# Kernel tuning notes

Hardware: AMD Instinct MI355X
Metric: run time of the kernel (lower is better)

## Reference

```python
import jax, jax.numpy as jnp
import numpy as np

N = 4096


def setup_inputs() -> dict:
    key = jax.random.key(0)
    ks = jax.random.split(key, 24)

    def idx(k, n, cols):
        base = jax.random.randint(k, (n,), 0, N)
        return jnp.stack([(base + j) % N for j in range(cols)], axis=1).astype(jnp.int32)

    x = jax.random.normal(ks[0], (N, 3), jnp.float32) * 3.0  # spread points so min pair dist is not tiny
    bond = idx(ks[1], 6144, 2)
    kb = jax.random.uniform(ks[2], (6144,), jnp.float32)
    b0 = jax.random.uniform(ks[3], (6144,), jnp.float32)
    angle = idx(ks[4], 8192, 3)
    kt = jax.random.uniform(ks[5], (8192,), jnp.float32)
    t0 = jax.random.uniform(ks[6], (8192,), jnp.float32) * 180.0  # degrees
    ureybradley = idx(ks[7], 4096, 2)
    ku = jax.random.uniform(ks[8], (4096,), jnp.float32)
    s0 = jax.random.uniform(ks[9], (4096,), jnp.float32)
    dihedral = idx(ks[10], 12288, 4)
    kd = jax.random.uniform(ks[11], (12288,), jnp.float32)
    nd = jax.random.randint(ks[12], (12288,), 1, 4).astype(jnp.float32)  # multiplicity
    d0 = jax.random.uniform(ks[13], (12288,), jnp.float32) * 360.0
    improper = idx(ks[14], 2048, 4)
    kp = jax.random.uniform(ks[15], (2048,), jnp.float32)
    p0 = jax.random.uniform(ks[16], (2048,), jnp.float32) * 180.0
    eps_ij = jax.random.uniform(ks[17], (N, N), jnp.float32)
    rmin_ij = jax.random.uniform(ks[18], (N, N), jnp.float32) * 0.5
    kqq_ij = jax.random.normal(ks[19], (N, N), jnp.float32)
    return dict(x=x, kb=kb, b0=b0, kt=kt, t0=t0, ku=ku, s0=s0, kd=kd, nd=nd, d0=d0,
                kp=kp, p0=p0, eps_ij=eps_ij, rmin_ij=rmin_ij, kqq_ij=kqq_ij,
                bond=bond, angle=angle, ureybradley=ureybradley,
                dihedral=dihedral, improper=improper, central=0)


def _torsion(x, quad):
    # signed dihedral angle for [M,4] index quadruples
    ab = x[quad[:, 1]] - x[quad[:, 0]]
    bc = x[quad[:, 2]] - x[quad[:, 1]]
    cd = x[quad[:, 3]] - x[quad[:, 2]]
    n1 = jnp.cross(ab, bc)
    n2 = jnp.cross(bc, cd)
    cos_d = jnp.sum(n1 * n2, axis=1) / (jnp.linalg.norm(n1, axis=1) * jnp.linalg.norm(n2, axis=1))
    ang = jnp.arccos(jnp.clip(cos_d, -0.9999, 0.9999))
    return ang * jnp.sign(jnp.sum(jnp.cross(n1, n2) * bc, axis=1))


def _energy(x, kb, b0, kt, t0, ku, s0, kd, nd, d0, kp, p0,
            eps_ij, rmin_ij, kqq_ij, bond, angle, ureybradley, dihedral, improper, central):
    # bonds
    dis = jnp.linalg.norm(x[bond[:, 0]] - x[bond[:, 1]], axis=1)
    V_bond = jnp.sum(kb * (dis - b0) ** 2)
    # angles
    ba = x[angle[:, 0]] - x[angle[:, 1]]
    bc = x[angle[:, 2]] - x[angle[:, 1]]
    cos_t = jnp.sum(ba * bc, axis=1) / (jnp.linalg.norm(ba, axis=1) * jnp.linalg.norm(bc, axis=1))
    theta = jnp.arccos(jnp.clip(cos_t, -0.9999, 0.9999))
    V_angle = jnp.sum(kt * (theta - jnp.deg2rad(t0)) ** 2)
    # Urey-Bradley 1-3 terms
    dub = jnp.linalg.norm(x[ureybradley[:, 0]] - x[ureybradley[:, 1]], axis=1)
    V_ub = jnp.sum(ku * (dub - s0) ** 2)
    # proper dihedrals
    delta = _torsion(x, dihedral)
    V_dih = jnp.sum(kd * (1.0 + jnp.cos(nd * delta - jnp.deg2rad(d0))))
    # impropers (harmonic)
    psi = _torsion(x, improper)
    V_imp = jnp.sum(kp * (psi - jnp.deg2rad(p0)) ** 2)
    # nonbonded: cdist(x,x) + I, summed over strict upper triangle
    n = x.shape[0]
    sq = jnp.sum(x * x, axis=1)
    d2 = jnp.maximum(sq[:, None] + sq[None, :] - 2.0 * (x @ x.T), 1e-12)
    eye = jnp.eye(n, dtype=bool)
    dist = jnp.sqrt(jnp.where(eye, 1.0, d2))  # diag -> 1, matching cdist + eye
    rod = rmin_ij / dist
    vdw = eps_ij * (rod ** 12 - 2.0 * rod ** 6)
    mask = jnp.triu(jnp.ones((n, n), bool), 1)
    V_vdw = jnp.sum(jnp.where(mask, vdw, 0.0))
    V_ele = jnp.sum(jnp.where(mask, kqq_ij / dist, 0.0))
    V = V_bond + V_angle + V_ub + V_dih + V_imp + V_vdw + V_ele
    if central:
        V = V + jnp.sum(0.1 * jnp.sum((x - jnp.mean(x, axis=0)) ** 2, axis=1))
    return V


def reference(x, kb, b0, kt, t0, ku, s0, kd, nd, d0, kp, p0,
              eps_ij, rmin_ij, kqq_ij, bond, angle, ureybradley, dihedral, improper, central):
    return _energy(x, kb, b0, kt, t0, ku, s0, kd, nd, d0, kp, p0,
                   eps_ij, rmin_ij, kqq_ij, bond, angle, ureybradley, dihedral, improper, central)
```

## Files before the change

### kernel.cpp

```cpp
#include <hip/hip_runtime.h>

#define NATOM   4096
#define NG4     (NATOM / 4)
#define NBOND   6144
#define NANGLE  8192
#define NUB     4096
#define NDIH    12288
#define NIMP    2048

#define NB_BLOCKS   2048
#define BOND_ITEMS  (NBOND + NANGLE + NUB + NDIH + NIMP)
#define BOND_WORKB  (BOND_ITEMS / 256)
#define BOND_BLOCKS (BOND_WORKB + 1)
#define TOTAL_SLOTS (NB_BLOCKS + BOND_BLOCKS)

#define DEG2RAD 0.017453292519943295f

static __device__ __forceinline__ double block_reduce(double v, double* sm) {
    #pragma unroll
    for (int off = 32; off > 0; off >>= 1) v += __shfl_down(v, off, 64);
    const int lane = threadIdx.x & 63, wid = threadIdx.x >> 6;
    __syncthreads();
    if (lane == 0) sm[wid] = v;
    __syncthreads();
    double r = 0.0;
    if (threadIdx.x == 0) {
        const int nw = blockDim.x >> 6;
        for (int w = 0; w < nw; ++w) r += sm[w];
    }
    return r;
}

static __device__ __forceinline__ float pair_term(
    float xi0, float xi1, float xi2,
    float xj0, float xj1, float xj2,
    float e, float r, float q, bool valid)
{
    const float dx = xi0 - xj0, dy = xi1 - xj1, dz = xi2 - xj2;
    float d2 = fmaf(dx, dx, fmaf(dy, dy, dz * dz));
    d2 = fmaxf(d2, 1e-12f);
    float inv = rsqrtf(d2);
    const float t = inv * inv;
    inv = inv * fmaf(-0.5f * d2, t, 1.5f);
    const float rod = r * inv;
    const float r2 = rod * rod;
    const float r6 = r2 * r2 * r2;
    const float v = fmaf(e * r6, r6 - 2.0f, q * inv);
    return valid ? v : 0.0f;
}

__global__ __launch_bounds__(256) void nb_kernel(
    const float4* __restrict__ xv,
    const float4* __restrict__ eps,
    const float4* __restrict__ rmin,
    const float4* __restrict__ kqq,
    double* __restrict__ ws)
{
    __shared__ double sm[4];
    const float* __restrict__ xf = (const float*)xv;
    double acc = 0.0;
    #pragma unroll
    for (int half = 0; half < 2; ++half) {
        const int i = (half == 0) ? (int)blockIdx.x : (NATOM - 1 - (int)blockIdx.x);
        const float xi0 = xf[3*i], xi1 = xf[3*i+1], xi2 = xf[3*i+2];
        const int g0 = (i + 1) >> 2;
        const size_t rowbase = (size_t)i * NG4;
        for (int g = g0 + (int)threadIdx.x; g < NG4; g += 256) {
            const float4 e = eps [rowbase + g];
            const float4 r = rmin[rowbase + g];
            const float4 q = kqq [rowbase + g];
            const float4 xa = xv[3*g], xb = xv[3*g+1], xc = xv[3*g+2];
            const int j0 = 4 * g;
            float s;
            s  = pair_term(xi0,xi1,xi2, xa.x,xa.y,xa.z, e.x,r.x,q.x, j0+0 > i);
            s += pair_term(xi0,xi1,xi2, xa.w,xb.x,xb.y, e.y,r.y,q.y, j0+1 > i);
            s += pair_term(xi0,xi1,xi2, xb.z,xb.w,xc.x, e.z,r.z,q.z, j0+2 > i);
            s += pair_term(xi0,xi1,xi2, xc.y,xc.z,xc.w, e.w,r.w,q.w, j0+3 > i);
            acc += (double)s;
        }
    }
    const double tot = block_reduce(acc, sm);
    if (threadIdx.x == 0) ws[blockIdx.x] = tot;
}

static __device__ __forceinline__ float torsion(const float* __restrict__ x,
                                                int i0, int i1, int i2, int i3) {
    const float ax = x[3*i1] - x[3*i0], ay = x[3*i1+1] - x[3*i0+1], az = x[3*i1+2] - x[3*i0+2];
    const float bx = x[3*i2] - x[3*i1], by = x[3*i2+1] - x[3*i1+1], bz = x[3*i2+2] - x[3*i1+2];
    const float cx = x[3*i3] - x[3*i2], cy = x[3*i3+1] - x[3*i2+1], cz = x[3*i3+2] - x[3*i2+2];
    const float n1x = ay*bz - az*by, n1y = az*bx - ax*bz, n1z = ax*by - ay*bx;
    const float n2x = by*cz - bz*cy, n2y = bz*cx - bx*cz, n2z = bx*cy - by*cx;
    const float dt  = n1x*n2x + n1y*n2y + n1z*n2z;
    const float nn1 = sqrtf(n1x*n1x + n1y*n1y + n1z*n1z);
    const float nn2 = sqrtf(n2x*n2x + n2y*n2y + n2z*n2z);
    float c = dt / (nn1 * nn2);
    c = fminf(fmaxf(c, -0.9999f), 0.9999f);
    const float ang = acosf(c);
    const float sx = n1y*n2z - n1z*n2y, sy = n1z*n2x - n1x*n2z, sz = n1x*n2y - n1y*n2x;
    const float s = sx*bx + sy*by + sz*bz;
    const float sg = (s > 0.0f) ? 1.0f : ((s < 0.0f) ? -1.0f : 0.0f);
    return ang * sg;
}

__global__ __launch_bounds__(256) void bonded_kernel(
    const float* __restrict__ x,
    const float* __restrict__ kb, const float* __restrict__ b0,
    const float* __restrict__ kt, const float* __restrict__ t0,
    const float* __restrict__ ku, const float* __restrict__ s0,
    const float* __restrict__ kd, const float* __restrict__ nd, const float* __restrict__ d0,
    const float* __restrict__ kp, const float* __restrict__ p0,
    const int* __restrict__ bond, const int* __restrict__ angle,
    const int* __restrict__ ub,   const int* __restrict__ dih,
    const int* __restrict__ imp,  const int* __restrict__ central,
    double* __restrict__ ws)
{
    __shared__ double sm[4];

    if (blockIdx.x == BOND_WORKB) {
        double out = 0.0;
        if (*central != 0) {
            double sx = 0.0, sy = 0.0, sz = 0.0, s2 = 0.0;
            for (int i = threadIdx.x; i < NATOM; i += 256) {
                const float a = x[3*i], b = x[3*i+1], c = x[3*i+2];
                sx += a; sy += b; sz += c;
                s2 += (double)a*a + (double)b*b + (double)c*c;
            }
            const double rx = block_reduce(sx, sm);
            const double ry = block_reduce(sy, sm);
            const double rz = block_reduce(sz, sm);
            const double r2 = block_reduce(s2, sm);
            if (threadIdx.x == 0)
                out = 0.1 * (r2 - (rx*rx + ry*ry + rz*rz) / (double)NATOM);
        }
        if (threadIdx.x == 0) ws[NB_BLOCKS + blockIdx.x] = out;
        return;
    }

    const int t = (int)blockIdx.x * 256 + (int)threadIdx.x;
    double v = 0.0;

    if (t < NBOND) {
        const int m = t;
        const int i = bond[2*m], j = bond[2*m+1];
        const float dx = x[3*i]-x[3*j], dy = x[3*i+1]-x[3*j+1], dz = x[3*i+2]-x[3*j+2];
        const float dis = sqrtf(dx*dx + dy*dy + dz*dz);
        const float d = dis - b0[m];
        v = (double)(kb[m] * d * d);
    } else if (t < NBOND + NANGLE) {
        const int m = t - NBOND;
        const int i = angle[3*m], j = angle[3*m+1], k = angle[3*m+2];
        const float bax = x[3*i]-x[3*j], bay = x[3*i+1]-x[3*j+1], baz = x[3*i+2]-x[3*j+2];
        const float bcx = x[3*k]-x[3*j], bcy = x[3*k+1]-x[3*j+1], bcz = x[3*k+2]-x[3*j+2];
        const float dt  = bax*bcx + bay*bcy + baz*bcz;
        const float na  = sqrtf(bax*bax + bay*bay + baz*baz);
        const float nb  = sqrtf(bcx*bcx + bcy*bcy + bcz*bcz);
        float c = dt / (na * nb);
        c = fminf(fmaxf(c, -0.9999f), 0.9999f);
        const float theta = acosf(c);
        const float d = theta - t0[m] * DEG2RAD;
        v = (double)(kt[m] * d * d);
    } else if (t < NBOND + NANGLE + NUB) {
        const int m = t - NBOND - NANGLE;
        const int i = ub[2*m], j = ub[2*m+1];
        const float dx = x[3*i]-x[3*j], dy = x[3*i+1]-x[3*j+1], dz = x[3*i+2]-x[3*j+2];
        const float dis = sqrtf(dx*dx + dy*dy + dz*dz);
        const float d = dis - s0[m];
        v = (double)(ku[m] * d * d);
    } else if (t < NBOND + NANGLE + NUB + NDIH) {
        const int m = t - NBOND - NANGLE - NUB;
        const float delta = torsion(x, dih[4*m], dih[4*m+1], dih[4*m+2], dih[4*m+3]);
        v = (double)(kd[m] * (1.0f + cosf(nd[m] * delta - d0[m] * DEG2RAD)));
    } else {
        const int m = t - NBOND - NANGLE - NUB - NDIH;
        const float psi = torsion(x, imp[4*m], imp[4*m+1], imp[4*m+2], imp[4*m+3]);
        const float d = psi - p0[m] * DEG2RAD;
        v = (double)(kp[m] * d * d);
    }

    const double tot = block_reduce(v, sm);
    if (threadIdx.x == 0) ws[NB_BLOCKS + blockIdx.x] = tot;
}

__global__ __launch_bounds__(256) void finalize_kernel(const double* __restrict__ ws,
                                                       float* __restrict__ out) {
    __shared__ double sm[4];
    double v = 0.0;
    for (int i = threadIdx.x; i < TOTAL_SLOTS; i += 256) v += ws[i];
    const double tot = block_reduce(v, sm);
    if (threadIdx.x == 0) out[0] = (float)tot;
}

extern "C" void kernel_launch(void* const* d_in, const int* in_sizes, int n_in,
                              void* d_out, int out_size, void* d_ws, size_t ws_size,
                              hipStream_t stream) {
    const float* x    = (const float*)d_in[0];
    const float* kb   = (const float*)d_in[1];
    const float* b0   = (const float*)d_in[2];
    const float* kt   = (const float*)d_in[3];
    const float* t0   = (const float*)d_in[4];
    const float* ku   = (const float*)d_in[5];
    const float* s0   = (const float*)d_in[6];
    const float* kd   = (const float*)d_in[7];
    const float* nd   = (const float*)d_in[8];
    const float* d0   = (const float*)d_in[9];
    const float* kp   = (const float*)d_in[10];
    const float* p0   = (const float*)d_in[11];
    const float* eps  = (const float*)d_in[12];
    const float* rmin = (const float*)d_in[13];
    const float* kqq  = (const float*)d_in[14];
    const int* bond   = (const int*)d_in[15];
    const int* angle  = (const int*)d_in[16];
    const int* ub     = (const int*)d_in[17];
    const int* dih    = (const int*)d_in[18];
    const int* imp    = (const int*)d_in[19];
    const int* cent   = (const int*)d_in[20];

    double* ws = (double*)d_ws;

    nb_kernel<<<NB_BLOCKS, 256, 0, stream>>>((const float4*)x, (const float4*)eps,
                                             (const float4*)rmin, (const float4*)kqq, ws);
    bonded_kernel<<<BOND_BLOCKS, 256, 0, stream>>>(x, kb, b0, kt, t0, ku, s0,
                                                   kd, nd, d0, kp, p0,
                                                   bond, angle, ub, dih, imp, cent, ws);
    finalize_kernel<<<1, 256, 0, stream>>>(ws, (float*)d_out);
}
```

Baseline: 218.8 us.

## Fuse nonbonded and bonded kernels, flatten paired-row work into fixed per-thread loads

Merges the nonbonded and bonded energy kernels into one launch, where the first block range handles nonbonded row pairs and the rest handles bonded terms. Each nonbonded block now concatenates its two rows (i and N-1-i) into one work list of about 1024 float4 groups. Each thread issues four independent loads up front, replacing the strided loop with its divergent tail. The aim is to remove a launch, balance work across threads and raise memory-level parallelism. One thread handles a single leftover group when the combined count is 1025.

```diff
diff --git a/kernel.cpp b/kernel.cpp
--- a/kernel.cpp
+++ b/kernel.cpp
@@ -49,38 +49,17 @@
     return valid ? v : 0.0f;
 }
 
-__global__ __launch_bounds__(256) void nb_kernel(
-    const float4* __restrict__ xv,
-    const float4* __restrict__ eps,
-    const float4* __restrict__ rmin,
-    const float4* __restrict__ kqq,
-    double* __restrict__ ws)
+static __device__ __forceinline__ float group_term(
+    int i, float xi0, float xi1, float xi2, int g,
+    float4 e, float4 r, float4 q, float4 xa, float4 xb, float4 xc)
 {
-    __shared__ double sm[4];
-    const float* __restrict__ xf = (const float*)xv;
-    double acc = 0.0;
-    #pragma unroll
-    for (int half = 0; half < 2; ++half) {
-        const int i = (half == 0) ? (int)blockIdx.x : (NATOM - 1 - (int)blockIdx.x);
-        const float xi0 = xf[3*i], xi1 = xf[3*i+1], xi2 = xf[3*i+2];
-        const int g0 = (i + 1) >> 2;
-        const size_t rowbase = (size_t)i * NG4;
-        for (int g = g0 + (int)threadIdx.x; g < NG4; g += 256) {
-            const float4 e = eps [rowbase + g];
-            const float4 r = rmin[rowbase + g];
-            const float4 q = kqq [rowbase + g];
-            const float4 xa = xv[3*g], xb = xv[3*g+1], xc = xv[3*g+2];
-            const int j0 = 4 * g;
-            float s;
-            s  = pair_term(xi0,xi1,xi2, xa.x,xa.y,xa.z, e.x,r.x,q.x, j0+0 > i);
-            s += pair_term(xi0,xi1,xi2, xa.w,xb.x,xb.y, e.y,r.y,q.y, j0+1 > i);
-            s += pair_term(xi0,xi1,xi2, xb.z,xb.w,xc.x, e.z,r.z,q.z, j0+2 > i);
-            s += pair_term(xi0,xi1,xi2, xc.y,xc.z,xc.w, e.w,r.w,q.w, j0+3 > i);
-            acc += (double)s;
-        }
-    }
-    const double tot = block_reduce(acc, sm);
-    if (threadIdx.x == 0) ws[blockIdx.x] = tot;
+    const int j0 = 4 * g;
+    float s;
+    s  = pair_term(xi0,xi1,xi2, xa.x,xa.y,xa.z, e.x,r.x,q.x, j0+0 > i);
+    s += pair_term(xi0,xi1,xi2, xa.w,xb.x,xb.y, e.y,r.y,q.y, j0+1 > i);
+    s += pair_term(xi0,xi1,xi2, xb.z,xb.w,xc.x, e.z,r.z,q.z, j0+2 > i);
+    s += pair_term(xi0,xi1,xi2, xc.y,xc.z,xc.w, e.w,r.w,q.w, j0+3 > i);
+    return s;
 }
 
 static __device__ __forceinline__ float torsion(const float* __restrict__ x,
@@ -102,8 +81,11 @@
     return ang * sg;
 }
 
-__global__ __launch_bounds__(256) void bonded_kernel(
-    const float* __restrict__ x,
+__global__ __launch_bounds__(256) void ff_kernel(
+    const float4* __restrict__ xv,
+    const float4* __restrict__ eps,
+    const float4* __restrict__ rmin,
+    const float4* __restrict__ kqq,
     const float* __restrict__ kb, const float* __restrict__ b0,
     const float* __restrict__ kt, const float* __restrict__ t0,
     const float* __restrict__ ku, const float* __restrict__ s0,
@@ -115,8 +97,62 @@
     double* __restrict__ ws)
 {
     __shared__ double sm[4];
-
-    if (blockIdx.x == BOND_WORKB) {
+    const float* __restrict__ x = (const float*)xv;
+
+    if (blockIdx.x < NB_BLOCKS) {
+        const int b  = (int)blockIdx.x;
+        const int i0 = b, i1 = NATOM - 1 - b;
+        const float xi00 = x[3*i0], xi01 = x[3*i0+1], xi02 = x[3*i0+2];
+        const float xi10 = x[3*i1], xi11 = x[3*i1+1], xi12 = x[3*i1+2];
+        const int ga = (i0 + 1) >> 2, gb = (i1 + 1) >> 2;
+        const int c0 = NG4 - ga;
+        const int c1 = NG4 - gb;
+        const int total = c0 + c1;
+        const int t = (int)threadIdx.x;
+
+        int  rw[4]; int gv[4]; bool lo[4];
+        #pragma unroll
+        for (int u = 0; u < 4; ++u) {
+            const int v = 4 * t + u;
+            lo[u] = v < c0;
+            rw[u] = lo[u] ? i0 : i1;
+            gv[u] = lo[u] ? (ga + v) : (gb + v - c0);
+        }
+        float4 le[4], lr[4], lq[4];
+        #pragma unroll
+        for (int u = 0; u < 4; ++u) {
+            const size_t base = (size_t)rw[u] * NG4 + gv[u];
+            le[u] = eps [base];
+            lr[u] = rmin[base];
+            lq[u] = kqq [base];
+        }
+        double acc = 0.0;
+        #pragma unroll
+        for (int u = 0; u < 4; ++u) {
+            const int g3 = 3 * gv[u];
+            const float4 xa = xv[g3], xb = xv[g3+1], xc = xv[g3+2];
+            const float xi0c = lo[u] ? xi00 : xi10;
+            const float xi1c = lo[u] ? xi01 : xi11;
+            const float xi2c = lo[u] ? xi02 : xi12;
+            acc += (double)group_term(rw[u], xi0c, xi1c, xi2c, gv[u],
+                                      le[u], lr[u], lq[u], xa, xb, xc);
+        }
+        if (t == 0 && total == 1025) {
+            const int g = gb + (1024 - c0);
+            const size_t base = (size_t)i1 * NG4 + g;
+            const int g3 = 3 * g;
+            acc += (double)group_term(i1, xi10, xi11, xi12, g,
+                                      eps[base], rmin[base], kqq[base],
+                                      xv[g3], xv[g3+1], xv[g3+2]);
+        }
+        const double tot = block_reduce(acc, sm);
+        if (t == 0) ws[blockIdx.x] = tot;
+        return;
+    }
+
+    const int bb = (int)blockIdx.x - NB_BLOCKS;
+
+    if (bb == BOND_WORKB) {
         double out = 0.0;
         if (*central != 0) {
             double sx = 0.0, sy = 0.0, sz = 0.0, s2 = 0.0;
@@ -132,11 +168,11 @@
             if (threadIdx.x == 0)
                 out = 0.1 * (r2 - (rx*rx + ry*ry + rz*rz) / (double)NATOM);
         }
-        if (threadIdx.x == 0) ws[NB_BLOCKS + blockIdx.x] = out;
+        if (threadIdx.x == 0) ws[NB_BLOCKS + bb] = out;
         return;
     }
 
-    const int t = (int)blockIdx.x * 256 + (int)threadIdx.x;
+    const int t = bb * 256 + (int)threadIdx.x;
     double v = 0.0;
 
     if (t < NBOND) {
@@ -178,7 +214,7 @@
     }
 
     const double tot = block_reduce(v, sm);
-    if (threadIdx.x == 0) ws[NB_BLOCKS + blockIdx.x] = tot;
+    if (threadIdx.x == 0) ws[NB_BLOCKS + bb] = tot;
 }
 
 __global__ __launch_bounds__(256) void finalize_kernel(const double* __restrict__ ws,
@@ -217,10 +253,9 @@
 
     double* ws = (double*)d_ws;
 
-    nb_kernel<<<NB_BLOCKS, 256, 0, stream>>>((const float4*)x, (const float4*)eps,
-                                             (const float4*)rmin, (const float4*)kqq, ws);
-    bonded_kernel<<<BOND_BLOCKS, 256, 0, stream>>>(x, kb, b0, kt, t0, ku, s0,
-                                                   kd, nd, d0, kp, p0,
-                                                   bond, angle, ub, dih, imp, cent, ws);
+    ff_kernel<<<NB_BLOCKS + BOND_BLOCKS, 256, 0, stream>>>(
+        (const float4*)x, (const float4*)eps, (const float4*)rmin, (const float4*)kqq,
+        kb, b0, kt, t0, ku, s0, kd, nd, d0, kp, p0,
+        bond, angle, ub, dih, imp, cent, ws);
     finalize_kernel<<<1, 256, 0, stream>>>(ws, (float*)d_out);
 }
```

Measured after the change: 225.5 us. +3.1%, slower.
